# Performance work log

Hardware: AMD Instinct MI355X
Metric: run time of the kernel (lower is better)

Reference implementation:

```python
import jax, jax.numpy as jnp
import numpy as np

IN_POINTS = 32
OUT_POINTS = 128
N_GROUPS = 4
EFF_IN = 64   # in_dim // n_groups
EFF_OUT = 64  # out_dim // n_groups
M_PARAMS = EFF_IN * EFF_OUT          # 4096
S_PARAMS = IN_POINTS * OUT_POINTS    # 4096
TOTAL = M_PARAMS + S_PARAMS          # 8192
EPS = 1e-5


def _ln2d(x):
    # LayerNorm over the last two dims, no affine (matches F.layer_norm(out, [P, C]))
    mu = jnp.mean(x, axis=(-2, -1), keepdims=True)
    var = jnp.mean(jnp.square(x - mu), axis=(-2, -1), keepdims=True)
    return (x - mu) * jax.lax.rsqrt(var + EPS)


def setup_inputs() -> dict:
    key = jax.random.key(0)
    ks = jax.random.split(key, 6)
    B, Q = 4, 900
    x = jax.random.normal(ks[0], (B, Q, N_GROUPS, IN_POINTS, EFF_IN), dtype=jnp.float32)
    query = jax.random.normal(ks[1], (B, Q, 256), dtype=jnp.float32)
    Wp = jax.random.normal(ks[2], (256, N_GROUPS * TOTAL), dtype=jnp.float32) * 0.02
    bp = jax.random.normal(ks[3], (N_GROUPS * TOTAL,), dtype=jnp.float32) * 0.02
    Wo = jax.random.normal(ks[4], (N_GROUPS * OUT_POINTS * EFF_OUT, 256), dtype=jnp.float32) * 0.02
    bo = jax.random.normal(ks[5], (256,), dtype=jnp.float32) * 0.02
    return {"x": x, "query": query, "Wp": Wp, "bp": bp, "Wo": Wo, "bo": bo}


def reference(x, query, Wp, bp, Wo, bo):
    B, Q, G, P, C = x.shape
    # generate mixing parameters: [B,Q,G*TOTAL] -> [B*Q, G, TOTAL]
    params = (query @ Wp + bp).reshape(B * Q, G, TOTAL)
    M = params[..., :M_PARAMS].reshape(B * Q, G, EFF_IN, EFF_OUT)
    S = params[..., M_PARAMS:].reshape(B * Q, G, OUT_POINTS, IN_POINTS)
    out = x.reshape(B * Q, G, P, C)
    # adaptive channel mixing: [n,g,P,C] @ [n,g,C,EFF_OUT]
    out = jnp.einsum('ngpc,ngco->ngpo', out, M)
    out = jax.nn.relu(_ln2d(out))
    # adaptive point mixing: [n,g,OUT_P,P] @ [n,g,P,EFF_OUT]
    out = jnp.einsum('ngqp,ngpo->ngqo', S, out)
    out = jax.nn.relu(_ln2d(out))
    # projection back to query dim + residual
    out = out.reshape(B, Q, G * OUT_POINTS * EFF_OUT) @ Wo + bo
    return query + out
```

## Files before the change

kernel.cpp:

```cpp
#include <hip/hip_runtime.h>
#include <stdint.h>


#define GQ 4
#define KQ 256
#define NP 32768
#define TOTAL_T 8192
#define MPAR 4096
#define INP 32
#define EIN 64
#define EOUT 64
#define BQT 3600
#define LN_EPS 1e-5f

typedef short s16x8 __attribute__((ext_vector_type(8)));
typedef float f32x4 __attribute__((ext_vector_type(4)));
typedef unsigned short u16;

__device__ __forceinline__ u16 f2bf(float f){
  union { float f; unsigned int u; } t; t.f = f;
  return (u16)((t.u + 0x7FFFu + ((t.u >> 16) & 1u)) >> 16);
}

__device__ __forceinline__ void gl16(const u16* g, u16* l){
  __builtin_amdgcn_global_load_lds(
      (const __attribute__((address_space(1))) unsigned int*)g,
      (__attribute__((address_space(3))) unsigned int*)l, 16, 0, 0);
}

__global__ __launch_bounds__(256) void cast_qr(const float* __restrict__ in,
                                               u16* __restrict__ out){
  int i = blockIdx.x * 256 + threadIdx.x;
  float4 f = *(const float4*)(in + 4 * (size_t)i);
  u16 v[4] = { f2bf(f.x), f2bf(f.y), f2bf(f.z), f2bf(f.w) };
  *(uint2*)(out + 4 * (size_t)i) = *(const uint2*)v;
}

__global__ __launch_bounds__(256) void transpose_cast(const float* __restrict__ in,
                                                      u16* __restrict__ out,
                                                      int R, int C){
  __shared__ float tile[32][33];
  int c0 = blockIdx.x * 32, r0 = blockIdx.y * 32;
  int tx = threadIdx.x, ty = threadIdx.y;
  #pragma unroll
  for (int i = 0; i < 32; i += 8)
    tile[ty + i][tx] = in[(size_t)(r0 + ty + i) * C + (c0 + tx)];
  __syncthreads();
  #pragma unroll
  for (int i = 0; i < 32; i += 8)
    out[(size_t)(c0 + ty + i) * R + (r0 + tx)] = f2bf(tile[tx][ty + i]);
}

__global__ __launch_bounds__(256) void gemm_params(
    const u16* __restrict__ qrb,
    const u16* __restrict__ WpT,
    const float* __restrict__ bp,
    u16* __restrict__ buf)
{
  __shared__ union SM {
    u16 AB[16384];
    u16 C[128 * 136];
  } sm;
  u16* As = sm.AB;
  u16* Bs = sm.AB + 8192;

  int n_base = blockIdx.x * 128;
  int m_base = blockIdx.y * 128;
  int t = threadIdx.x, wave = t >> 6, lane = t & 63, quad = lane >> 4, l15 = lane & 15;
  int mrow0 = (wave & 1) * 64, ncol0 = (wave >> 1) * 64;
  int srow = wave * 8 + (lane >> 3);
  int scol = (lane & 7) * 8;

  const f32x4 fz = {0.f, 0.f, 0.f, 0.f};
  f32x4 acc[4][4];
  #pragma unroll
  for (int i = 0; i < 4; i++)
    #pragma unroll
    for (int j = 0; j < 4; j++) acc[i][j] = fz;

  for (int ko = 0; ko < 4; ko++) {
    int k0 = ko * 64;
    #pragma unroll
    for (int i = 0; i < 4; i++) {
      int ar = m_base + i * 32 + srow; ar = ar < (BQT - 1) ? ar : (BQT - 1);
      gl16(qrb + (size_t)ar * KQ + k0 + scol, As + i * 2048 + wave * 512);
      int br = n_base + i * 32 + srow;
      gl16(WpT + (size_t)br * KQ + k0 + scol, Bs + i * 2048 + wave * 512);
    }
    __syncthreads();
    #pragma unroll
    for (int ks = 0; ks < 2; ks++) {
      s16x8 a[4], b[4];
      #pragma unroll
      for (int i = 0; i < 4; i++)
        a[i] = *(const s16x8*)(As + (mrow0 + i * 16 + l15) * 64 + ks * 32 + quad * 8);
      #pragma unroll
      for (int j = 0; j < 4; j++)
        b[j] = *(const s16x8*)(Bs + (ncol0 + j * 16 + l15) * 64 + ks * 32 + quad * 8);
      #pragma unroll
      for (int i = 0; i < 4; i++)
        #pragma unroll
        for (int j = 0; j < 4; j++)
          acc[i][j] = __builtin_amdgcn_mfma_f32_16x16x32_bf16(a[i], b[j], acc[i][j], 0, 0, 0);
    }
    __syncthreads();
  }

  #pragma unroll
  for (int j = 0; j < 4; j++) {
    int cl = ncol0 + j * 16 + l15;
    float bias = bp[n_base + cl];
    #pragma unroll
    for (int i = 0; i < 4; i++) {
      int rl = mrow0 + i * 16 + quad * 4;
      #pragma unroll
      for (int r = 0; r < 4; r++)
        sm.C[(rl + r) * 136 + cl] = f2bf(acc[i][j][r] + bias);
    }
  }
  __syncthreads();
  int c8 = (t & 15) * 8;
  #pragma unroll
  for (int it = 0; it < 8; it++) {
    int row = (t >> 4) + it * 16;
    int gr = m_base + row;
    s16x8 v = *(const s16x8*)(&sm.C[row * 136 + c8]);
    if (gr < BQT)
      *(s16x8*)(&buf[(size_t)gr * NP + n_base + c8]) = v;
  }
}

#define MTSW(o, c) ((c) ^ ((((o) >> 3) & 7) * 8))
__global__ __launch_bounds__(256) void mixer(
    const float* __restrict__ x,
    u16* __restrict__ buf)
{
  __shared__ u16 MT[64][72];
  __shared__ u16 H1[64][40];
  __shared__ u16 O2[128][72];
  __shared__ float redS[4], redQ[4];

  int bid = blockIdx.x;
  int nl = bid >> 2, g = bid & 3;
  int t = threadIdx.x, wave = t >> 6, lane = t & 63, quad = lane >> 4, l15 = lane & 15;
  u16* slice = buf + (size_t)nl * NP + g * TOTAL_T;
  const float* xs = x + ((size_t)nl * GQ + g) * (INP * EIN);

  s16x8 sfrag[2];
  #pragma unroll
  for (int mt = 0; mt < 2; mt++) {
    int qp = (wave * 2 + mt) * 16 + l15;
    sfrag[mt] = *(const s16x8*)(slice + MPAR + qp * INP + quad * 8);
  }
  s16x8 xfrag[2][2];
  #pragma unroll
  for (int nt = 0; nt < 2; nt++)
    #pragma unroll
    for (int ks = 0; ks < 2; ks++) {
      const float* src = xs + (nt * 16 + l15) * EIN + ks * 32 + quad * 8;
      float4 f0 = *(const float4*)(src);
      float4 f1 = *(const float4*)(src + 4);
      s16x8 v;
      v[0] = (short)f2bf(f0.x); v[1] = (short)f2bf(f0.y);
      v[2] = (short)f2bf(f0.z); v[3] = (short)f2bf(f0.w);
      v[4] = (short)f2bf(f1.x); v[5] = (short)f2bf(f1.y);
      v[6] = (short)f2bf(f1.z); v[7] = (short)f2bf(f1.w);
      xfrag[nt][ks] = v;
    }

  #pragma unroll
  for (int i = 0; i < 2; i++) {
    int ch = t + i * 256;
    int c = ch >> 3, o0 = (ch & 7) * 8;
    s16x8 v = *(const s16x8*)(slice + c * EOUT + o0);
    #pragma unroll
    for (int jj = 0; jj < 8; jj++) MT[o0 + jj][MTSW(o0 + jj, c)] = (u16)v[jj];
  }
  __syncthreads();

  const f32x4 fz = {0.f, 0.f, 0.f, 0.f};
  f32x4 acc1[2]; acc1[0] = fz; acc1[1] = fz;
  #pragma unroll
  for (int ks = 0; ks < 2; ks++) {
    int o = wave * 16 + l15;
    s16x8 a = *(const s16x8*)(&MT[o][MTSW(o, ks * 32 + quad * 8)]);
    acc1[0] = __builtin_amdgcn_mfma_f32_16x16x32_bf16(a, xfrag[0][ks], acc1[0], 0, 0, 0);
    acc1[1] = __builtin_amdgcn_mfma_f32_16x16x32_bf16(a, xfrag[1][ks], acc1[1], 0, 0, 0);
  }
  float s = 0.f, sq = 0.f;
  #pragma unroll
  for (int nt = 0; nt < 2; nt++)
    #pragma unroll
    for (int r = 0; r < 4; r++) { float v = acc1[nt][r]; s += v; sq += v * v; }
  #pragma unroll
  for (int off = 32; off >= 1; off >>= 1) { s += __shfl_xor(s, off); sq += __shfl_xor(sq, off); }
  if (lane == 0) { redS[wave] = s; redQ[wave] = sq; }
  __syncthreads();
  {
    float S1 = redS[0] + redS[1] + redS[2] + redS[3];
    float Q1 = redQ[0] + redQ[1] + redQ[2] + redQ[3];
    float mean = S1 * (1.f / 2048.f);
    float var = fmaxf(Q1 * (1.f / 2048.f) - mean * mean, 0.f);
    float rstd = rsqrtf(var + LN_EPS);
    #pragma unroll
    for (int nt = 0; nt < 2; nt++)
      #pragma unroll
      for (int r = 0; r < 4; r++) {
        float v = (acc1[nt][r] - mean) * rstd;
        v = v > 0.f ? v : 0.f;
        H1[wave * 16 + quad * 4 + r][nt * 16 + l15] = f2bf(v);
      }
  }
  __syncthreads();

  f32x4 acc2[2][4];
  #pragma unroll
  for (int mt = 0; mt < 2; mt++)
    #pragma unroll
    for (int nt = 0; nt < 4; nt++) acc2[mt][nt] = fz;
  #pragma unroll
  for (int nt = 0; nt < 4; nt++) {
    s16x8 b = *(const s16x8*)(&H1[nt * 16 + l15][quad * 8]);
    acc2[0][nt] = __builtin_amdgcn_mfma_f32_16x16x32_bf16(sfrag[0], b, acc2[0][nt], 0, 0, 0);
    acc2[1][nt] = __builtin_amdgcn_mfma_f32_16x16x32_bf16(sfrag[1], b, acc2[1][nt], 0, 0, 0);
  }
  s = 0.f; sq = 0.f;
  #pragma unroll
  for (int mt = 0; mt < 2; mt++)
    #pragma unroll
    for (int nt = 0; nt < 4; nt++)
      #pragma unroll
      for (int r = 0; r < 4; r++) { float v = acc2[mt][nt][r]; s += v; sq += v * v; }
  #pragma unroll
  for (int off = 32; off >= 1; off >>= 1) { s += __shfl_xor(s, off); sq += __shfl_xor(sq, off); }
  if (lane == 0) { redS[wave] = s; redQ[wave] = sq; }
  __syncthreads();
  {
    float S2 = redS[0] + redS[1] + redS[2] + redS[3];
    float Q2 = redQ[0] + redQ[1] + redQ[2] + redQ[3];
    float mean = S2 * (1.f / 8192.f);
    float var = fmaxf(Q2 * (1.f / 8192.f) - mean * mean, 0.f);
    float rstd = rsqrtf(var + LN_EPS);
    #pragma unroll
    for (int mt = 0; mt < 2; mt++)
      #pragma unroll
      for (int nt = 0; nt < 4; nt++)
        #pragma unroll
        for (int r = 0; r < 4; r++) {
          float v = (acc2[mt][nt][r] - mean) * rstd;
          v = v > 0.f ? v : 0.f;
          O2[(wave * 2 + mt) * 16 + quad * 4 + r][nt * 16 + l15] = f2bf(v);
        }
  }
  __syncthreads();
  #pragma unroll
  for (int i = 0; i < 4; i++) {
    int ch = t + i * 256;
    int qp = ch >> 3, o0 = (ch & 7) * 8;
    s16x8 v = *(const s16x8*)(&O2[qp][o0]);
    *(s16x8*)(slice + qp * EOUT + o0) = v;
  }
}

__global__ __launch_bounds__(256) void gemm_out(
    const u16* __restrict__ hid,
    const u16* __restrict__ WoT,
    float* __restrict__ part,
    int kslice)
{
  __shared__ u16 As[128 * 64];
  __shared__ u16 Bs[128 * 64];
  int n_base = blockIdx.x * 128;
  int m_base = blockIdx.y * 128;
  int ksl = blockIdx.z;
  int t = threadIdx.x, wave = t >> 6, lane = t & 63, quad = lane >> 4, l15 = lane & 15;
  int mrow0 = (wave & 1) * 64, ncol0 = (wave >> 1) * 64;
  int srow = wave * 8 + (lane >> 3);
  int scol = (lane & 7) * 8;

  const f32x4 fz = {0.f, 0.f, 0.f, 0.f};
  f32x4 acc[4][4];
  #pragma unroll
  for (int i = 0; i < 4; i++)
    #pragma unroll
    for (int j = 0; j < 4; j++) acc[i][j] = fz;

  int kbase = ksl * kslice;
  for (int ko = 0; ko < kslice / 64; ko++) {
    int k0 = kbase + ko * 64;
    #pragma unroll
    for (int i = 0; i < 4; i++) {
      int ar = m_base + i * 32 + srow; ar = ar < (BQT - 1) ? ar : (BQT - 1);
      gl16(hid + (size_t)ar * NP + k0 + scol, As + i * 2048 + wave * 512);
      int br = n_base + i * 32 + srow;
      gl16(WoT + (size_t)br * NP + k0 + scol, Bs + i * 2048 + wave * 512);
    }
    __syncthreads();
    #pragma unroll
    for (int ks = 0; ks < 2; ks++) {
      s16x8 a[4], b[4];
      #pragma unroll
      for (int i = 0; i < 4; i++)
        a[i] = *(const s16x8*)(As + (mrow0 + i * 16 + l15) * 64 + ks * 32 + quad * 8);
      #pragma unroll
      for (int j = 0; j < 4; j++)
        b[j] = *(const s16x8*)(Bs + (ncol0 + j * 16 + l15) * 64 + ks * 32 + quad * 8);
      #pragma unroll
      for (int i = 0; i < 4; i++)
        #pragma unroll
        for (int j = 0; j < 4; j++)
          acc[i][j] = __builtin_amdgcn_mfma_f32_16x16x32_bf16(a[i], b[j], acc[i][j], 0, 0, 0);
    }
    __syncthreads();
  }
  #pragma unroll
  for (int j = 0; j < 4; j++) {
    int colg = n_base + ncol0 + j * 16 + l15;
    #pragma unroll
    for (int i = 0; i < 4; i++) {
      int row0 = m_base + mrow0 + i * 16 + quad * 4;
      #pragma unroll
      for (int r = 0; r < 4; r++)
        if (row0 + r < BQT)
          part[((size_t)ksl * BQT + row0 + r) * 256 + colg] = acc[i][j][r];
    }
  }
}

__global__ __launch_bounds__(256) void reduce_out(
    const float* __restrict__ part, const float* __restrict__ qr,
    const float* __restrict__ bo, float* __restrict__ out, int KS)
{
  int nl = blockIdx.x, j = threadIdx.x;
  float s = bo[j] + qr[(size_t)nl * KQ + j];
  for (int ks = 0; ks < KS; ks++)
    s += part[((size_t)ks * BQT + nl) * 256 + j];
  out[(size_t)nl * KQ + j] = s;
}

extern "C" void kernel_launch(void* const* d_in, const int* in_sizes, int n_in,
                              void* d_out, int out_size, void* d_ws, size_t ws_size,
                              hipStream_t stream)
{
  (void)in_sizes; (void)n_in; (void)out_size;
  const float* x  = (const float*)d_in[0];
  const float* qr = (const float*)d_in[1];
  const float* Wp = (const float*)d_in[2];
  const float* bp = (const float*)d_in[3];
  const float* Wo = (const float*)d_in[4];
  const float* bo = (const float*)d_in[5];
  float* out = (float*)d_out;

  char* ws = (char*)d_ws;
  u16* WpT = (u16*)ws;
  u16* WoT = (u16*)(ws + 16777216);
  u16* buf = (u16*)(ws + 33554432);
  char* tail = ws + 33554432ull + (size_t)BQT * NP * 2ull;
  u16* qrb  = (u16*)tail;
  float* part = (float*)tail;

  size_t base = 33554432ull + (size_t)BQT * NP * 2ull;
  int KS = (ws_size >= base + 16ull * BQT * 256 * 4) ? 16 : 8;
  int kslice = NP / KS;

  cast_qr<<<dim3(BQT * KQ / 1024), 256, 0, stream>>>(qr, qrb);
  transpose_cast<<<dim3(NP / 32, KQ / 32), dim3(32, 8), 0, stream>>>(Wp, WpT, KQ, NP);
  transpose_cast<<<dim3(KQ / 32, NP / 32), dim3(32, 8), 0, stream>>>(Wo, WoT, NP, KQ);

  gemm_params<<<dim3(NP / 128, 29), 256, 0, stream>>>(qrb, WpT, bp, buf);
  mixer<<<dim3(BQT * GQ), 256, 0, stream>>>(x, buf);
  gemm_out<<<dim3(2, 29, KS), 256, 0, stream>>>(buf, WoT, part, kslice);
  reduce_out<<<dim3(BQT), 256, 0, stream>>>(part, qr, bo, out, KS);
}
```

Measured before the change: 579.7 us.

## Load GEMM operands directly to registers with double-buffered prefetch, drop LDS staging

```diff
diff --git a/kernel.cpp b/kernel.cpp
--- a/kernel.cpp
+++ b/kernel.cpp
@@ -22,12 +22,6 @@
   return (u16)((t.u + 0x7FFFu + ((t.u >> 16) & 1u)) >> 16);
 }
 
-__device__ __forceinline__ void gl16(const u16* g, u16* l){
-  __builtin_amdgcn_global_load_lds(
-      (const __attribute__((address_space(1))) unsigned int*)g,
-      (__attribute__((address_space(3))) unsigned int*)l, 16, 0, 0);
-}
-
 __global__ __launch_bounds__(256) void cast_qr(const float* __restrict__ in,
                                                u16* __restrict__ out){
   int i = blockIdx.x * 256 + threadIdx.x;
@@ -51,25 +45,26 @@
     out[(size_t)(c0 + ty + i) * R + (r0 + tx)] = f2bf(tile[tx][ty + i]);
 }
 
-__global__ __launch_bounds__(256) void gemm_params(
+__global__ __launch_bounds__(256, 2) void gemm_params(
     const u16* __restrict__ qrb,
     const u16* __restrict__ WpT,
     const float* __restrict__ bp,
     u16* __restrict__ buf)
 {
-  __shared__ union SM {
-    u16 AB[16384];
-    u16 C[128 * 136];
-  } sm;
-  u16* As = sm.AB;
-  u16* Bs = sm.AB + 8192;
-
+  __shared__ u16 C[128 * 136];
   int n_base = blockIdx.x * 128;
   int m_base = blockIdx.y * 128;
   int t = threadIdx.x, wave = t >> 6, lane = t & 63, quad = lane >> 4, l15 = lane & 15;
   int mrow0 = (wave & 1) * 64, ncol0 = (wave >> 1) * 64;
-  int srow = wave * 8 + (lane >> 3);
-  int scol = (lane & 7) * 8;
+
+  const u16* ap[4]; const u16* bpt[4];
+  #pragma unroll
+  for (int i = 0; i < 4; i++) {
+    int ar = m_base + mrow0 + i * 16 + l15; ar = ar < BQT ? ar : (BQT - 1);
+    ap[i] = qrb + (size_t)ar * KQ + quad * 8;
+    int br = n_base + ncol0 + i * 16 + l15;
+    bpt[i] = WpT + (size_t)br * KQ + quad * 8;
+  }
 
   const f32x4 fz = {0.f, 0.f, 0.f, 0.f};
   f32x4 acc[4][4];
@@ -78,32 +73,46 @@
     #pragma unroll
     for (int j = 0; j < 4; j++) acc[i][j] = fz;
 
-  for (int ko = 0; ko < 4; ko++) {
-    int k0 = ko * 64;
+  s16x8 a[2][4], b[2][4], an[2][4], bn[2][4];
+  #pragma unroll
+  for (int ks = 0; ks < 2; ks++)
     #pragma unroll
     for (int i = 0; i < 4; i++) {
-      int ar = m_base + i * 32 + srow; ar = ar < (BQT - 1) ? ar : (BQT - 1);
-      gl16(qrb + (size_t)ar * KQ + k0 + scol, As + i * 2048 + wave * 512);
-      int br = n_base + i * 32 + srow;
-      gl16(WpT + (size_t)br * KQ + k0 + scol, Bs + i * 2048 + wave * 512);
+      a[ks][i] = *(const s16x8*)(ap[i] + ks * 32);
+      b[ks][i] = *(const s16x8*)(bpt[i] + ks * 32);
     }
-    __syncthreads();
-    #pragma unroll
-    for (int ks = 0; ks < 2; ks++) {
-      s16x8 a[4], b[4];
-      #pragma unroll
-      for (int i = 0; i < 4; i++)
-        a[i] = *(const s16x8*)(As + (mrow0 + i * 16 + l15) * 64 + ks * 32 + quad * 8);
-      #pragma unroll
-      for (int j = 0; j < 4; j++)
-        b[j] = *(const s16x8*)(Bs + (ncol0 + j * 16 + l15) * 64 + ks * 32 + quad * 8);
+  #pragma unroll
+  for (int ko = 0; ko < 4; ko += 2) {
+    int k1 = (ko + 1) * 64;
+    int k2 = (ko + 2 < 4 ? ko + 2 : 3) * 64;
+    #pragma unroll
+    for (int ks = 0; ks < 2; ks++)
+      #pragma unroll
+      for (int i = 0; i < 4; i++) {
+        an[ks][i] = *(const s16x8*)(ap[i] + k1 + ks * 32);
+        bn[ks][i] = *(const s16x8*)(bpt[i] + k1 + ks * 32);
+      }
+    #pragma unroll
+    for (int ks = 0; ks < 2; ks++)
       #pragma unroll
       for (int i = 0; i < 4; i++)
         #pragma unroll
         for (int j = 0; j < 4; j++)
-          acc[i][j] = __builtin_amdgcn_mfma_f32_16x16x32_bf16(a[i], b[j], acc[i][j], 0, 0, 0);
-    }
-    __syncthreads();
+          acc[i][j] = __builtin_amdgcn_mfma_f32_16x16x32_bf16(a[ks][i], b[ks][j], acc[i][j], 0, 0, 0);
+    #pragma unroll
+    for (int ks = 0; ks < 2; ks++)
+      #pragma unroll
+      for (int i = 0; i < 4; i++) {
+        a[ks][i] = *(const s16x8*)(ap[i] + k2 + ks * 32);
+        b[ks][i] = *(const s16x8*)(bpt[i] + k2 + ks * 32);
+      }
+    #pragma unroll
+    for (int ks = 0; ks < 2; ks++)
+      #pragma unroll
+      for (int i = 0; i < 4; i++)
+        #pragma unroll
+        for (int j = 0; j < 4; j++)
+          acc[i][j] = __builtin_amdgcn_mfma_f32_16x16x32_bf16(an[ks][i], bn[ks][j], acc[i][j], 0, 0, 0);
   }
 
   #pragma unroll
@@ -115,7 +124,7 @@
       int rl = mrow0 + i * 16 + quad * 4;
       #pragma unroll
       for (int r = 0; r < 4; r++)
-        sm.C[(rl + r) * 136 + cl] = f2bf(acc[i][j][r] + bias);
+        C[(rl + r) * 136 + cl] = f2bf(acc[i][j][r] + bias);
     }
   }
   __syncthreads();
@@ -124,7 +133,7 @@
   for (int it = 0; it < 8; it++) {
     int row = (t >> 4) + it * 16;
     int gr = m_base + row;
-    s16x8 v = *(const s16x8*)(&sm.C[row * 136 + c8]);
+    s16x8 v = *(const s16x8*)(&C[row * 136 + c8]);
     if (gr < BQT)
       *(s16x8*)(&buf[(size_t)gr * NP + n_base + c8]) = v;
   }
@@ -262,21 +271,26 @@
   }
 }
 
-__global__ __launch_bounds__(256) void gemm_out(
+__global__ __launch_bounds__(256, 2) void gemm_out(
     const u16* __restrict__ hid,
     const u16* __restrict__ WoT,
     float* __restrict__ part,
     int kslice)
 {
-  __shared__ u16 As[128 * 64];
-  __shared__ u16 Bs[128 * 64];
   int n_base = blockIdx.x * 128;
   int m_base = blockIdx.y * 128;
   int ksl = blockIdx.z;
   int t = threadIdx.x, wave = t >> 6, lane = t & 63, quad = lane >> 4, l15 = lane & 15;
   int mrow0 = (wave & 1) * 64, ncol0 = (wave >> 1) * 64;
-  int srow = wave * 8 + (lane >> 3);
-  int scol = (lane & 7) * 8;
+
+  const u16* ap[4]; const u16* bpt[4];
+  #pragma unroll
+  for (int i = 0; i < 4; i++) {
+    int ar = m_base + mrow0 + i * 16 + l15; ar = ar < BQT ? ar : (BQT - 1);
+    ap[i] = hid + (size_t)ar * NP + quad * 8;
+    int br = n_base + ncol0 + i * 16 + l15;
+    bpt[i] = WoT + (size_t)br * NP + quad * 8;
+  }
 
   const f32x4 fz = {0.f, 0.f, 0.f, 0.f};
   f32x4 acc[4][4];
@@ -286,32 +300,47 @@
     for (int j = 0; j < 4; j++) acc[i][j] = fz;
 
   int kbase = ksl * kslice;
-  for (int ko = 0; ko < kslice / 64; ko++) {
-    int k0 = kbase + ko * 64;
+  int nko = kslice / 64;
+
+  s16x8 a[2][4], b[2][4], an[2][4], bn[2][4];
+  #pragma unroll
+  for (int ks = 0; ks < 2; ks++)
     #pragma unroll
     for (int i = 0; i < 4; i++) {
-      int ar = m_base + i * 32 + srow; ar = ar < (BQT - 1) ? ar : (BQT - 1);
-      gl16(hid + (size_t)ar * NP + k0 + scol, As + i * 2048 + wave * 512);
-      int br = n_base + i * 32 + srow;
-      gl16(WoT + (size_t)br * NP + k0 + scol, Bs + i * 2048 + wave * 512);
+      a[ks][i] = *(const s16x8*)(ap[i] + kbase + ks * 32);
+      b[ks][i] = *(const s16x8*)(bpt[i] + kbase + ks * 32);
     }
-    __syncthreads();
-    #pragma unroll
-    for (int ks = 0; ks < 2; ks++) {
-      s16x8 a[4], b[4];
-      #pragma unroll
-      for (int i = 0; i < 4; i++)
-        a[i] = *(const s16x8*)(As + (mrow0 + i * 16 + l15) * 64 + ks * 32 + quad * 8);
-      #pragma unroll
-      for (int j = 0; j < 4; j++)
-        b[j] = *(const s16x8*)(Bs + (ncol0 + j * 16 + l15) * 64 + ks * 32 + quad * 8);
+  for (int ko = 0; ko < nko; ko += 2) {
+    int k1 = kbase + (ko + 1) * 64;
+    int k2 = kbase + (ko + 2 < nko ? ko + 2 : nko - 1) * 64;
+    #pragma unroll
+    for (int ks = 0; ks < 2; ks++)
+      #pragma unroll
+      for (int i = 0; i < 4; i++) {
+        an[ks][i] = *(const s16x8*)(ap[i] + k1 + ks * 32);
+        bn[ks][i] = *(const s16x8*)(bpt[i] + k1 + ks * 32);
+      }
+    #pragma unroll
+    for (int ks = 0; ks < 2; ks++)
       #pragma unroll
       for (int i = 0; i < 4; i++)
         #pragma unroll
         for (int j = 0; j < 4; j++)
-          acc[i][j] = __builtin_amdgcn_mfma_f32_16x16x32_bf16(a[i], b[j], acc[i][j], 0, 0, 0);
-    }
-    __syncthreads();
+          acc[i][j] = __builtin_amdgcn_mfma_f32_16x16x32_bf16(a[ks][i], b[ks][j], acc[i][j], 0, 0, 0);
+    #pragma unroll
+    for (int ks = 0; ks < 2; ks++)
+      #pragma unroll
+      for (int i = 0; i < 4; i++) {
+        a[ks][i] = *(const s16x8*)(ap[i] + k2 + ks * 32);
+        b[ks][i] = *(const s16x8*)(bpt[i] + k2 + ks * 32);
+      }
+    #pragma unroll
+    for (int ks = 0; ks < 2; ks++)
+      #pragma unroll
+      for (int i = 0; i < 4; i++)
+        #pragma unroll
+        for (int j = 0; j < 4; j++)
+          acc[i][j] = __builtin_amdgcn_mfma_f32_16x16x32_bf16(an[ks][i], bn[ks][j], acc[i][j], 0, 0, 0);
   }
   #pragma unroll
   for (int j = 0; j < 4; j++) {
```

Result: slower. 780.2 us (+34.6%).
